# Optimization experiments

Measured on AMD Instinct MI355X. Metric: run time of the kernel, lower is better.

## Reference

```python
import jax, jax.numpy as jnp
import numpy as np

# camera / raster constants
N = 10000            # gaussians
W = 256
H = 256
FX = 200.0
FY = 200.0
TILE = 16
NTX = W // TILE
NTY = H // TILE
NT = NTX * NTY       # 256 tiles
P = TILE * TILE      # 256 pixels per tile
K = 256              # max gaussians kept per tile
NEAR = 0.3
MAGIC = 1.2          # frustum expansion factor from project_culling
LP = 0.3 / (FX * FX) # low-pass filter added to 2D covariance diagonal


def quat_to_rot(q):
    w, x, y, z = q[:, 0], q[:, 1], q[:, 2], q[:, 3]
    r0 = jnp.stack([1 - 2 * (y * y + z * z), 2 * (x * y - w * z), 2 * (x * z + w * y)], -1)
    r1 = jnp.stack([2 * (x * y + w * z), 1 - 2 * (x * x + z * z), 2 * (y * z - w * x)], -1)
    r2 = jnp.stack([2 * (x * z - w * y), 2 * (y * z + w * x), 1 - 2 * (x * x + y * y)], -1)
    return jnp.stack([r0, r1, r2], axis=1)  # [N,3,3]


def splat_forward(pos, rgb, opacity, quaternion, scale, w2c_r, w2c_t):
    # ---- project + frustum cull (global_culling) ----
    q = quaternion / jnp.linalg.norm(quaternion, axis=-1, keepdims=True)
    R = quat_to_rot(q)
    sigma = jnp.exp(scale)                               # normalize_scale
    cov3d = jnp.einsum('nij,nj,nkj->nik', R, sigma * sigma, R)
    p_cam = pos @ w2c_r.T + w2c_t                        # [N,3]
    x, y, z = p_cam[:, 0], p_cam[:, 1], p_cam[:, 2]
    zc = jnp.maximum(z, 1e-6)
    half_w = W * MAGIC / 2 / FX
    half_h = H * MAGIC / 2 / FY
    mean2d = jnp.stack([x / zc, y / zc], -1)             # camera-plane coords
    in_frustum = (z > NEAR) & (jnp.abs(mean2d[:, 0]) < half_w) & (jnp.abs(mean2d[:, 1]) < half_h)
    iz = 1.0 / zc
    zero = jnp.zeros_like(iz)
    J = jnp.stack([jnp.stack([iz, zero, -x * iz * iz], -1),
                   jnp.stack([zero, iz, -y * iz * iz], -1)], axis=1)  # [N,2,3]
    cov_cam = jnp.einsum('ij,njk,lk->nil', w2c_r, cov3d, w2c_r)
    cov2d = jnp.einsum('nij,njk,nlk->nil', J, cov_cam, J)            # [N,2,2]
    a = cov2d[:, 0, 0] + LP
    c = cov2d[:, 1, 1] + LP
    b = cov2d[:, 0, 1]

    # ---- per-tile culling + fixed-K binning (calc_tile_list / gather_gaussians) ----
    cx = (jnp.arange(NTX) * TILE + TILE / 2 - W / 2) / FX
    cy = (jnp.arange(NTY) * TILE + TILE / 2 - H / 2) / FY
    centers = jnp.stack(jnp.meshgrid(cx, cy, indexing='xy'), -1).reshape(NT, 2)  # [NT,2] (ty-major)
    tile_half_diag = 0.5 * jnp.sqrt((TILE / FX) ** 2 + (TILE / FY) ** 2)
    mid = 0.5 * (a + c)
    sigma_max = jnp.sqrt(jnp.maximum(mid + jnp.sqrt(jnp.maximum((0.5 * (a - c)) ** 2 + b * b, 0.0)), 1e-12))
    dist = jnp.linalg.norm(centers[:, None, :] - mean2d[None, :, :], axis=-1)   # [NT,N]
    valid = in_frustum[None, :] & (dist <= (3.0 * sigma_max + tile_half_diag)[None, :])
    score = jnp.where(valid, -dist, -1e10)
    vals, idx = jax.lax.top_k(score, K)                                          # [NT,K]
    valid_k = vals > -1e9

    mean_g = mean2d[idx]                     # [NT,K,2]
    z_g = z[idx]
    a_g, b_g, c_g = a[idx], b[idx], c[idx]
    opa_g = jax.nn.sigmoid(opacity)[idx]
    rgb_g = jax.nn.sigmoid(rgb)[idx]         # [NT,K,3]

    # ---- depth sort within each tile ----
    order = jnp.argsort(jnp.where(valid_k, z_g, jnp.inf), axis=-1)
    def srt(arr):
        o = order.reshape(order.shape + (1,) * (arr.ndim - 2))
        return jnp.take_along_axis(arr, o, axis=1)
    mean_s, a_s, b_s, c_s = srt(mean_g), srt(a_g), srt(b_g), srt(c_g)
    opa_s, rgb_s = srt(opa_g), srt(rgb_g)
    valid_s = srt(valid_k).astype(pos.dtype)

    # ---- per-pixel front-to-back alpha compositing (draw) ----
    px = ((jnp.arange(W) + 0.5 - W / 2) / FX).reshape(NTX, TILE)
    py = ((jnp.arange(H) + 0.5 - H / 2) / FY).reshape(NTY, TILE)
    U = jnp.broadcast_to(px[None, :, None, :], (NTY, NTX, TILE, TILE)).reshape(NT, P)
    V = jnp.broadcast_to(py[:, None, :, None], (NTY, NTX, TILE, TILE)).reshape(NT, P)
    dx = U[:, :, None] - mean_s[:, None, :, 0]          # [NT,P,K]
    dy = V[:, :, None] - mean_s[:, None, :, 1]
    det = jnp.maximum(a_s * c_s - b_s * b_s, 1e-12)[:, None, :]
    maha = (c_s[:, None, :] * dx * dx - 2.0 * b_s[:, None, :] * dx * dy + a_s[:, None, :] * dy * dy) / det
    alpha = jnp.clip(opa_s[:, None, :] * jnp.exp(-0.5 * maha), 0.0, 0.99) * valid_s[:, None, :]
    trans = jnp.cumprod(1.0 - alpha, axis=-1)
    texc = jnp.concatenate([jnp.ones_like(trans[..., :1]), trans[..., :-1]], axis=-1)
    color = jnp.einsum('tpk,tkc->tpc', alpha * texc, rgb_s)  # [NT,P,3]
    img = color.reshape(NTY, NTX, TILE, TILE, 3).transpose(0, 2, 1, 3, 4).reshape(H, W, 3)
    return jnp.clip(img, 0.0, 1.0)


def setup_inputs() -> dict:
    key = jax.random.key(0)
    ks = jax.random.split(key, 6)
    zpos = jax.random.uniform(ks[0], (N,), minval=2.0, maxval=6.0)
    uv = jax.random.uniform(ks[1], (N, 2), minval=-0.6, maxval=0.6)
    pos = jnp.concatenate([uv * zpos[:, None], zpos[:, None]], axis=-1)
    rgb = jax.random.normal(ks[2], (N, 3))              # pre-sigmoid logits
    opacity = jax.random.normal(ks[3], (N,)) + 1.5      # sigmoid -> ~0.8 like init_opacity
    quaternion = jax.random.normal(ks[4], (N, 4))
    scale = 0.2 * jax.random.normal(ks[5], (N, 3)) - 4.5  # exp -> ~0.01 world sigma
    w2c_r = jnp.eye(3, dtype=jnp.float32)
    w2c_t = jnp.zeros((3,), dtype=jnp.float32)
    return {"pos": pos, "rgb": rgb, "opacity": opacity, "quaternion": quaternion,
            "scale": scale, "w2c_r": w2c_r, "w2c_t": w2c_t}


def reference(pos, rgb, opacity, quaternion, scale, w2c_r, w2c_t):
    return splat_forward(pos, rgb, opacity, quaternion, scale, w2c_r, w2c_t)
```

## Files before the change

### kernel.cpp

```cpp
#include <hip/hip_runtime.h>
#include <math.h>

namespace {
constexpr int W = 256, H = 256, TILE = 16, NTX = 16, NT = 256, K = 256;
constexpr float FX = 200.0f, FY = 200.0f, NEARP = 0.3f, MAGIC = 1.2f;
constexpr float LP = 0.3f / (FX * FX);
constexpr float HALF_W = W * MAGIC / 2.0f / FX;
constexpr float HALF_H = H * MAGIC / 2.0f / FY;
constexpr float THDIAG = 0.05656854249492381f;
constexpr int CAP = 2048;
constexpr int N_PAD = 10240;
constexpr int BT = 1024;
constexpr int NB_MAX = 64;
constexpr int SEG = 256;
constexpr size_t A_OFF  = 0;
constexpr size_t B_OFF  = A_OFF + (size_t)N_PAD * 16;
constexpr size_t C_OFF  = B_OFF + (size_t)N_PAD * 16;
constexpr size_t SL_OFF = C_OFF + (size_t)N_PAD * 16;
constexpr size_t LD_OFF = SL_OFF + (size_t)NT * NB_MAX * 4;
constexpr size_t LZ_OFF = LD_OFF + (size_t)NT * NB_MAX * SEG * 8;
constexpr size_t WS_FULL = LZ_OFF + (size_t)NT * NB_MAX * SEG * 8;
}

struct Pre { float mx, my, z, a, b, c, radius; };

__device__ inline Pre preprocess(int g, const float* __restrict__ pos,
                                 const float* __restrict__ quat,
                                 const float* __restrict__ scl,
                                 const float* __restrict__ w2cr,
                                 const float* __restrict__ w2ct) {
  float p0 = pos[3*g+0], p1 = pos[3*g+1], p2 = pos[3*g+2];
  float qw = quat[4*g+0], qx = quat[4*g+1], qy = quat[4*g+2], qz = quat[4*g+3];
  float inv = 1.0f / sqrtf(qw*qw + qx*qx + qy*qy + qz*qz);
  qw *= inv; qx *= inv; qy *= inv; qz *= inv;
  float r00 = 1.f-2.f*(qy*qy+qz*qz), r01 = 2.f*(qx*qy-qw*qz), r02 = 2.f*(qx*qz+qw*qy);
  float r10 = 2.f*(qx*qy+qw*qz), r11 = 1.f-2.f*(qx*qx+qz*qz), r12 = 2.f*(qy*qz-qw*qx);
  float r20 = 2.f*(qx*qz-qw*qy), r21 = 2.f*(qy*qz+qw*qx), r22 = 1.f-2.f*(qx*qx+qy*qy);
  float e0 = expf(scl[3*g+0]); float s0 = e0*e0;
  float e1 = expf(scl[3*g+1]); float s1 = e1*e1;
  float e2 = expf(scl[3*g+2]); float s2 = e2*e2;
  float C00 = r00*r00*s0 + r01*r01*s1 + r02*r02*s2;
  float C01 = r00*r10*s0 + r01*r11*s1 + r02*r12*s2;
  float C02 = r00*r20*s0 + r01*r21*s1 + r02*r22*s2;
  float C11 = r10*r10*s0 + r11*r11*s1 + r12*r12*s2;
  float C12 = r10*r20*s0 + r11*r21*s1 + r12*r22*s2;
  float C22 = r20*r20*s0 + r21*r21*s1 + r22*r22*s2;
  float w00=w2cr[0],w01=w2cr[1],w02=w2cr[2];
  float w10=w2cr[3],w11=w2cr[4],w12=w2cr[5];
  float w20=w2cr[6],w21=w2cr[7],w22=w2cr[8];
  float x = w00*p0 + w01*p1 + w02*p2 + w2ct[0];
  float y = w10*p0 + w11*p1 + w12*p2 + w2ct[1];
  float z = w20*p0 + w21*p1 + w22*p2 + w2ct[2];
  float m00 = w00*C00 + w01*C01 + w02*C02;
  float m01 = w00*C01 + w01*C11 + w02*C12;
  float m02 = w00*C02 + w01*C12 + w02*C22;
  float m10 = w10*C00 + w11*C01 + w12*C02;
  float m11 = w10*C01 + w11*C11 + w12*C12;
  float m12 = w10*C02 + w11*C12 + w12*C22;
  float m20 = w20*C00 + w21*C01 + w22*C02;
  float m21 = w20*C01 + w21*C11 + w22*C12;
  float m22 = w20*C02 + w21*C12 + w22*C22;
  float v00 = m00*w00 + m01*w01 + m02*w02;
  float v01 = m00*w10 + m01*w11 + m02*w12;
  float v02 = m00*w20 + m01*w21 + m02*w22;
  float v10 = m10*w00 + m11*w01 + m12*w02;
  float v11 = m10*w10 + m11*w11 + m12*w12;
  float v12 = m10*w20 + m11*w21 + m12*w22;
  float v20 = m20*w00 + m21*w01 + m22*w02;
  float v21 = m20*w10 + m21*w11 + m22*w12;
  float v22 = m20*w20 + m21*w21 + m22*w22;
  float zc = fmaxf(z, 1e-6f);
  float iz = 1.0f / zc;
  float mx = x * iz, my = y * iz;
  float iz2 = iz * iz;
  float jx = -x * iz2, jy = -y * iz2;
  float a00 = iz*v00 + jx*v20, a01 = iz*v01 + jx*v21, a02 = iz*v02 + jx*v22;
  float a10 = iz*v10 + jy*v20, a11 = iz*v11 + jy*v21, a12 = iz*v12 + jy*v22;
  float A  = a00*iz + a02*jx + LP;
  float Bv = a01*iz + a02*jy;
  float Cv = a11*iz + a12*jy + LP;
  float mid = 0.5f*(A + Cv);
  float hh  = 0.5f*(A - Cv);
  float disc = fmaxf(hh*hh + Bv*Bv, 0.0f);
  float smax = sqrtf(fmaxf(mid + sqrtf(disc), 1e-12f));
  bool infr = (z > NEARP) && (fabsf(mx) < HALF_W) && (fabsf(my) < HALF_H);
  Pre r;
  r.mx = mx; r.my = my; r.z = z; r.a = A; r.b = Bv; r.c = Cv;
  r.radius = infr ? (3.0f * smax + THDIAG) : -1.0f;
  return r;
}


template <bool BIN>
__global__ __launch_bounds__(256)
void pre_bin(const float* __restrict__ pos, const float* __restrict__ rgb,
             const float* __restrict__ opac, const float* __restrict__ quat,
             const float* __restrict__ scl, const float* __restrict__ w2cr,
             const float* __restrict__ w2ct,
             float4* __restrict__ pa, float4* __restrict__ pb,
             float4* __restrict__ pc, int* __restrict__ seglen,
             unsigned long long* __restrict__ listd,
             unsigned long long* __restrict__ listz, int n) {
  __shared__ int s_tc[NT];
  const int tid = (int)threadIdx.x;
  const int blk = (int)blockIdx.x;
  if (BIN) {
    if (tid < NT) s_tc[tid] = 0;
    __syncthreads();
  }
  const int g = blk * 256 + tid;
  if (g < n) {
    Pre p = preprocess(g, pos, quat, scl, w2cr, w2ct);
    float det = fmaxf(p.a * p.c - p.b * p.b, 1e-12f);
    pa[g] = make_float4(p.mx, p.my, p.radius, p.z);
    pb[g] = make_float4(p.a, p.b, p.c, 1.0f / det);
    pc[g] = make_float4(1.0f / (1.0f + __expf(-opac[g])),
                        1.0f / (1.0f + __expf(-rgb[3*g+0])),
                        1.0f / (1.0f + __expf(-rgb[3*g+1])),
                        1.0f / (1.0f + __expf(-rgb[3*g+2])));
    if (BIN && p.radius >= 0.0f) {
      float r = p.radius;
      int txlo = max(0,     (int)floorf(((p.mx - r) * FX + 120.0f) * 0.0625f));
      int txhi = min(NTX-1, (int)ceilf (((p.mx + r) * FX + 120.0f) * 0.0625f));
      int tylo = max(0,     (int)floorf(((p.my - r) * FY + 120.0f) * 0.0625f));
      int tyhi = min(NTX-1, (int)ceilf (((p.my + r) * FY + 120.0f) * 0.0625f));
      unsigned long long gbits = (unsigned int)g;
      for (int ty = tylo; ty <= tyhi; ++ty) {
        float cy = (ty * TILE + TILE * 0.5f - H * 0.5f) / FY;
        float ddy = cy - p.my;
        for (int tx = txlo; tx <= txhi; ++tx) {
          float cx = (tx * TILE + TILE * 0.5f - W * 0.5f) / FX;
          float ddx = cx - p.mx;
          float dist = sqrtf(ddx * ddx + ddy * ddy);
          if (dist <= r) {
            int t = ty * NTX + tx;
            int slot = atomicAdd(&s_tc[t], 1);
            size_t idx = ((size_t)t * NB_MAX + blk) * SEG + slot;
            listd[idx] = ((unsigned long long)__float_as_uint(dist) << 32) | gbits;
            listz[idx] = ((unsigned long long)__float_as_uint(p.z)  << 32) | gbits;
          }
        }
      }
    }
  }
  if (BIN) {
    __syncthreads();
    if (tid < NT) seglen[(size_t)tid * NB_MAX + blk] = s_tc[tid];
  }
}


template <int S>
__device__ inline void hsortN(unsigned long long* key, int M) {
  const int tid = (int)threadIdx.x;
  __syncthreads();
  unsigned long long e[S];
  #pragma unroll
  for (int s = 0; s < S; ++s) {
    int i = tid + (s << 10);
    e[s] = (i < M) ? key[i] : ~0ull;
  }
  for (int k = 2; k <= M; k <<= 1) {
    for (int j = k >> 1; j >= 64; j >>= 1) {
      __syncthreads();
      #pragma unroll
      for (int s = 0; s < S; ++s) {
        int i = tid + (s << 10);
        if (i < M) key[i] = e[s];
      }
      __syncthreads();
      #pragma unroll
      for (int s = 0; s < S; ++s) {
        int i = tid + (s << 10);
        if (i < M) {
          unsigned long long p = key[i ^ j];
          bool takeMin = (((i & j) == 0) == ((i & k) == 0));
          e[s] = ((p < e[s]) == takeMin) ? p : e[s];
        }
      }
    }
    int j0 = ((k >> 1) < 32) ? (k >> 1) : 32;
    for (int j = j0; j >= 1; j >>= 1) {
      #pragma unroll
      for (int s = 0; s < S; ++s) {
        int i = tid + (s << 10);
        unsigned long long p = __shfl_xor(e[s], j, 64);
        bool takeMin = (((i & j) == 0) == ((i & k) == 0));
        e[s] = ((p < e[s]) == takeMin) ? p : e[s];
      }
    }
  }
  __syncthreads();
  #pragma unroll
  for (int s = 0; s < S; ++s) {
    int i = tid + (s << 10);
    if (i < M) key[i] = e[s];
  }
  __syncthreads();
}


__device__ inline void sort_blend_store(
    const float4* __restrict__ pa, const float4* __restrict__ pb,
    const float4* __restrict__ pc, float* __restrict__ out,
    unsigned long long* s_zkey, int* s_rank,
    float4* s_p0, float4* s_p1, float2* s_p2, float4* s_part,
    int cnt2, int tx, int ty) {
  const int tid = (int)threadIdx.x;
  {
    const int e = tid & 255;
    const int q = tid >> 8;
    if (e < cnt2) {
      unsigned long long mykey = s_zkey[e];
      int jlo = q * 64;
      int jhi = min(cnt2, jlo + 64);
      int partial = 0;
      for (int j = jlo; j < jhi; ++j)
        partial += (s_zkey[j] < mykey) ? 1 : 0;
      if (partial) atomicAdd(&s_rank[e], partial);
    }
  }
  __syncthreads();
  if (tid < cnt2) {
    int g = (int)(s_zkey[tid] & 0xffffffffu);
    int r = s_rank[tid];
    float4 A = pa[g], B = pb[g], C = pc[g];
    s_p0[r] = make_float4(A.x, A.y, B.x, B.y);
    s_p1[r] = make_float4(B.z, B.w, C.x, C.y);
    s_p2[r] = make_float2(C.z, C.w);
  }
  __syncthreads();
  const int p    = tid & 255;
  const int q    = tid >> 8;
  const int prow = p / TILE, pcol = p % TILE;
  const float u = ((float)(tx * TILE + pcol) + 0.5f - W * 0.5f) / FX;
  const float v = ((float)(ty * TILE + prow) + 0.5f - H * 0.5f) / FY;
  const int chunk = (cnt2 + 3) >> 2;
  const int k0 = q * chunk;
  const int k1 = min(cnt2, k0 + chunk);
  float T = 1.0f, accr = 0.0f, accg = 0.0f, accb = 0.0f;
  for (int k2 = k0; k2 < k1; ++k2) {
    float4 p0 = s_p0[k2];
    float4 p1 = s_p1[k2];
    float2 p2 = s_p2[k2];
    float dx = u - p0.x;
    float dy = v - p0.y;
    float maha = (p1.x*dx*dx - 2.0f*p0.w*dx*dy + p0.z*dy*dy) * p1.y;
    float alpha = fminf(p1.z * __expf(-0.5f * maha), 0.99f);
    float w = alpha * T;
    accr += w * p1.w;
    accg += w * p2.x;
    accb += w * p2.y;
    T *= (1.0f - alpha);
  }
  s_part[tid] = make_float4(accr, accg, accb, T);
  __syncthreads();
  if (q == 0) {
    float4 P0 = s_part[p];
    float4 P1 = s_part[p + 256];
    float4 P2 = s_part[p + 512];
    float4 P3 = s_part[p + 768];
    float r = P0.x + P0.w * (P1.x + P1.w * (P2.x + P2.w * P3.x));
    float g = P0.y + P0.w * (P1.y + P1.w * (P2.y + P2.w * P3.y));
    float b = P0.z + P0.w * (P1.z + P1.w * (P2.z + P2.w * P3.z));
    const int row = ty * TILE + prow;
    const int col = tx * TILE + pcol;
    const int o = (row * W + col) * 3;
    out[o+0] = fminf(fmaxf(r, 0.0f), 1.0f);
    out[o+1] = fminf(fmaxf(g, 0.0f), 1.0f);
    out[o+2] = fminf(fmaxf(b, 0.0f), 1.0f);
  }
}


__global__ __launch_bounds__(BT)
void render_list(const float4* __restrict__ pa, const float4* __restrict__ pb,
                 const float4* __restrict__ pc, const int* __restrict__ seglen,
                 const unsigned long long* __restrict__ listd,
                 const unsigned long long* __restrict__ listz,
                 float* __restrict__ out, int nb) {
  __shared__ unsigned long long s_dkey[CAP];
  __shared__ unsigned long long s_zkey[CAP];
  __shared__ int s_off[NB_MAX + 1];
  __shared__ int s_rank[K];
  __shared__ float4 s_p0[K];
  __shared__ float4 s_p1[K];
  __shared__ float2 s_p2[K];
  __shared__ float4 s_part[BT];

  const int t  = (int)blockIdx.x;
  const int tx = t % NTX;
  const int ty = t / NTX;
  const int tid = (int)threadIdx.x;

  if (tid < K) s_rank[tid] = 0;
  if (tid < 64) {
    int v = (tid < nb) ? seglen[(size_t)t * NB_MAX + tid] : 0;
    #pragma unroll
    for (int d = 1; d < 64; d <<= 1) {
      int u2 = __shfl_up(v, d, 64);
      if (tid >= d) v += u2;
    }
    if (tid == 0) s_off[0] = 0;
    if (tid < nb) s_off[tid + 1] = v;
  }
  __syncthreads();
  int cnt = min(s_off[nb], CAP);

  for (int i = tid; i < cnt; i += BT) {
    int lo = 0, hi = nb;
    while (hi - lo > 1) {
      int mid = (lo + hi) >> 1;
      if (s_off[mid] <= i) lo = mid; else hi = mid;
    }
    size_t src = ((size_t)t * NB_MAX + lo) * SEG + (size_t)(i - s_off[lo]);
    s_dkey[i] = listd[src];
    s_zkey[i] = listz[src];
  }
  __syncthreads();
  int cnt2 = cnt;

  if (cnt > K) {
    int M = 512; while (M < cnt) M <<= 1;
    for (int i = cnt + tid; i < M; i += BT) s_dkey[i] = ~0ull;
    if (M <= 1024) hsortN<1>(s_dkey, M);
    else           hsortN<2>(s_dkey, 2048);
    if (tid < K) {
      int g = (int)(s_dkey[tid] & 0xffffffffu);
      s_zkey[tid] = ((unsigned long long)__float_as_uint(pa[g].w) << 32) |
                    (unsigned int)g;
    }
    __syncthreads();
    cnt2 = K;
  }

  sort_blend_store(pa, pb, pc, out, s_zkey, s_rank, s_p0, s_p1, s_p2, s_part,
                   cnt2, tx, ty);
}


__global__ __launch_bounds__(BT)
void render_scan(const float4* __restrict__ pa, const float4* __restrict__ pb,
                 const float4* __restrict__ pc, float* __restrict__ out, int n) {
  __shared__ unsigned long long s_dkey[CAP];
  __shared__ unsigned long long s_zkey[CAP];
  __shared__ int s_rank[K];
  __shared__ float4 s_p0[K];
  __shared__ float4 s_p1[K];
  __shared__ float2 s_p2[K];
  __shared__ float4 s_part[BT];
  __shared__ int s_cnt;

  const int t  = (int)blockIdx.x;
  const int tx = t % NTX;
  const int ty = t / NTX;
  const int tid = (int)threadIdx.x;
  const int lane = tid & 63;
  const float cxc = (tx * TILE + TILE * 0.5f - W * 0.5f) / FX;
  const float cyc = (ty * TILE + TILE * 0.5f - H * 0.5f) / FY;

  if (tid == 0) s_cnt = 0;
  if (tid < K) s_rank[tid] = 0;
  __syncthreads();

  for (int g = tid; g < n; g += BT) {
    float4 v = pa[g];
    float ddx = cxc - v.x, ddy = cyc - v.y;
    float dist = sqrtf(ddx * ddx + ddy * ddy);
    bool hit = (v.z >= 0.0f) && (dist <= v.z);
    unsigned long long m = __ballot(hit);
    if (m) {
      int leader = __ffsll((long long)m) - 1;
      int base = 0;
      if (lane == leader) base = atomicAdd(&s_cnt, __popcll(m));
      base = __shfl(base, leader, 64);
      if (hit) {
        int slot = base + __popcll(m & ((1ull << lane) - 1ull));
        if (slot < CAP) {
          s_dkey[slot] = ((unsigned long long)__float_as_uint(dist) << 32) |
                         (unsigned int)g;
          s_zkey[slot] = ((unsigned long long)__float_as_uint(v.w) << 32) |
                         (unsigned int)g;
        }
      }
    }
  }
  __syncthreads();
  int cnt = min(s_cnt, CAP);
  int cnt2 = cnt;

  if (cnt > K) {
    int M = 512; while (M < cnt) M <<= 1;
    for (int i = cnt + tid; i < M; i += BT) s_dkey[i] = ~0ull;
    if (M <= 1024) hsortN<1>(s_dkey, M);
    else           hsortN<2>(s_dkey, 2048);
    if (tid < K) {
      int g = (int)(s_dkey[tid] & 0xffffffffu);
      s_zkey[tid] = ((unsigned long long)__float_as_uint(pa[g].w) << 32) |
                    (unsigned int)g;
    }
    __syncthreads();
    cnt2 = K;
  }

  sort_blend_store(pa, pb, pc, out, s_zkey, s_rank, s_p0, s_p1, s_p2, s_part,
                   cnt2, tx, ty);
}

extern "C" void kernel_launch(void* const* d_in, const int* in_sizes, int n_in,
                              void* d_out, int out_size, void* d_ws, size_t ws_size,
                              hipStream_t stream) {
  const float* pos  = (const float*)d_in[0];
  const float* rgb  = (const float*)d_in[1];
  const float* opac = (const float*)d_in[2];
  const float* quat = (const float*)d_in[3];
  const float* scl  = (const float*)d_in[4];
  const float* w2cr = (const float*)d_in[5];
  const float* w2ct = (const float*)d_in[6];
  float* out = (float*)d_out;
  const int n = in_sizes[0] / 3;
  const int nb = (n + 255) / 256;

  char* ws = (char*)d_ws;
  float4* pa = (float4*)(ws + A_OFF);
  float4* pb = (float4*)(ws + B_OFF);
  float4* pc = (float4*)(ws + C_OFF);
  int* seglen = (int*)(ws + SL_OFF);
  unsigned long long* listd = (unsigned long long*)(ws + LD_OFF);
  unsigned long long* listz = (unsigned long long*)(ws + LZ_OFF);

  if (ws_size >= WS_FULL && nb <= NB_MAX) {
    pre_bin<true><<<nb, 256, 0, stream>>>(
        pos, rgb, opac, quat, scl, w2cr, w2ct, pa, pb, pc, seglen, listd, listz, n);
    render_list<<<NT, BT, 0, stream>>>(pa, pb, pc, seglen, listd, listz, out, nb);
  } else {
    pre_bin<false><<<nb, 256, 0, stream>>>(
        pos, rgb, opac, quat, scl, w2cr, w2ct, pa, pb, pc, seglen, listd, listz, n);
    render_scan<<<NT, BT, 0, stream>>>(pa, pb, pc, out, n);
  }
}
```

Measured before the change: 24.99 us.

## Fuse preprocess/binning and tile render into one cooperative kernel with grid sync

```diff
diff --git a/kernel.cpp b/kernel.cpp
--- a/kernel.cpp
+++ b/kernel.cpp
@@ -1,5 +1,8 @@
 #include <hip/hip_runtime.h>
+#include <hip/hip_cooperative_groups.h>
 #include <math.h>
+
+namespace cg = cooperative_groups;
 
 namespace {
 constexpr int W = 256, H = 256, TILE = 16, NTX = 16, NT = 256, K = 256;
@@ -8,7 +11,7 @@
 constexpr float HALF_W = W * MAGIC / 2.0f / FX;
 constexpr float HALF_H = H * MAGIC / 2.0f / FY;
 constexpr float THDIAG = 0.05656854249492381f;
-constexpr int CAP = 2048;
+constexpr int CAP = 1024;
 constexpr int N_PAD = 10240;
 constexpr int BT = 1024;
 constexpr int NB_MAX = 64;
@@ -90,117 +93,83 @@
   return r;
 }
 
-
 template <bool BIN>
-__global__ __launch_bounds__(256)
-void pre_bin(const float* __restrict__ pos, const float* __restrict__ rgb,
-             const float* __restrict__ opac, const float* __restrict__ quat,
-             const float* __restrict__ scl, const float* __restrict__ w2cr,
-             const float* __restrict__ w2ct,
-             float4* __restrict__ pa, float4* __restrict__ pb,
-             float4* __restrict__ pc, int* __restrict__ seglen,
-             unsigned long long* __restrict__ listd,
-             unsigned long long* __restrict__ listz, int n) {
-  __shared__ int s_tc[NT];
-  const int tid = (int)threadIdx.x;
-  const int blk = (int)blockIdx.x;
-  if (BIN) {
-    if (tid < NT) s_tc[tid] = 0;
-    __syncthreads();
-  }
-  const int g = blk * 256 + tid;
-  if (g < n) {
-    Pre p = preprocess(g, pos, quat, scl, w2cr, w2ct);
-    float det = fmaxf(p.a * p.c - p.b * p.b, 1e-12f);
-    pa[g] = make_float4(p.mx, p.my, p.radius, p.z);
-    pb[g] = make_float4(p.a, p.b, p.c, 1.0f / det);
-    pc[g] = make_float4(1.0f / (1.0f + __expf(-opac[g])),
-                        1.0f / (1.0f + __expf(-rgb[3*g+0])),
-                        1.0f / (1.0f + __expf(-rgb[3*g+1])),
-                        1.0f / (1.0f + __expf(-rgb[3*g+2])));
-    if (BIN && p.radius >= 0.0f) {
-      float r = p.radius;
-      int txlo = max(0,     (int)floorf(((p.mx - r) * FX + 120.0f) * 0.0625f));
-      int txhi = min(NTX-1, (int)ceilf (((p.mx + r) * FX + 120.0f) * 0.0625f));
-      int tylo = max(0,     (int)floorf(((p.my - r) * FY + 120.0f) * 0.0625f));
-      int tyhi = min(NTX-1, (int)ceilf (((p.my + r) * FY + 120.0f) * 0.0625f));
-      unsigned long long gbits = (unsigned int)g;
-      for (int ty = tylo; ty <= tyhi; ++ty) {
-        float cy = (ty * TILE + TILE * 0.5f - H * 0.5f) / FY;
-        float ddy = cy - p.my;
-        for (int tx = txlo; tx <= txhi; ++tx) {
-          float cx = (tx * TILE + TILE * 0.5f - W * 0.5f) / FX;
-          float ddx = cx - p.mx;
-          float dist = sqrtf(ddx * ddx + ddy * ddy);
-          if (dist <= r) {
-            int t = ty * NTX + tx;
-            int slot = atomicAdd(&s_tc[t], 1);
-            size_t idx = ((size_t)t * NB_MAX + blk) * SEG + slot;
-            listd[idx] = ((unsigned long long)__float_as_uint(dist) << 32) | gbits;
-            listz[idx] = ((unsigned long long)__float_as_uint(p.z)  << 32) | gbits;
-          }
+__device__ inline void pre_one(int g, int blk, const float* __restrict__ pos,
+                               const float* __restrict__ rgb,
+                               const float* __restrict__ opac,
+                               const float* __restrict__ quat,
+                               const float* __restrict__ scl,
+                               const float* __restrict__ w2cr,
+                               const float* __restrict__ w2ct,
+                               float4* __restrict__ pa, float4* __restrict__ pb,
+                               float4* __restrict__ pc,
+                               unsigned long long* __restrict__ listd,
+                               unsigned long long* __restrict__ listz,
+                               int* s_tc) {
+  Pre p = preprocess(g, pos, quat, scl, w2cr, w2ct);
+  float det = fmaxf(p.a * p.c - p.b * p.b, 1e-12f);
+  pa[g] = make_float4(p.mx, p.my, p.radius, p.z);
+  pb[g] = make_float4(p.a, p.b, p.c, 1.0f / det);
+  pc[g] = make_float4(1.0f / (1.0f + __expf(-opac[g])),
+                      1.0f / (1.0f + __expf(-rgb[3*g+0])),
+                      1.0f / (1.0f + __expf(-rgb[3*g+1])),
+                      1.0f / (1.0f + __expf(-rgb[3*g+2])));
+  if (BIN && p.radius >= 0.0f) {
+    float r = p.radius;
+    int txlo = max(0,     (int)floorf(((p.mx - r) * FX + 120.0f) * 0.0625f));
+    int txhi = min(NTX-1, (int)ceilf (((p.mx + r) * FX + 120.0f) * 0.0625f));
+    int tylo = max(0,     (int)floorf(((p.my - r) * FY + 120.0f) * 0.0625f));
+    int tyhi = min(NTX-1, (int)ceilf (((p.my + r) * FY + 120.0f) * 0.0625f));
+    unsigned long long gbits = (unsigned int)g;
+    for (int ty = tylo; ty <= tyhi; ++ty) {
+      float cy = (ty * TILE + TILE * 0.5f - H * 0.5f) / FY;
+      float ddy = cy - p.my;
+      for (int tx = txlo; tx <= txhi; ++tx) {
+        float cx = (tx * TILE + TILE * 0.5f - W * 0.5f) / FX;
+        float ddx = cx - p.mx;
+        float dist = sqrtf(ddx * ddx + ddy * ddy);
+        if (dist <= r) {
+          int t = ty * NTX + tx;
+          int slot = atomicAdd(&s_tc[t], 1);
+          size_t idx = ((size_t)t * NB_MAX + blk) * SEG + slot;
+          listd[idx] = ((unsigned long long)__float_as_uint(dist) << 32) | gbits;
+          listz[idx] = ((unsigned long long)__float_as_uint(p.z)  << 32) | gbits;
         }
       }
     }
   }
-  if (BIN) {
-    __syncthreads();
-    if (tid < NT) seglen[(size_t)tid * NB_MAX + blk] = s_tc[tid];
-  }
-}
-
-
-template <int S>
-__device__ inline void hsortN(unsigned long long* key, int M) {
+}
+
+
+__device__ inline void hsort1(unsigned long long* key, int M) {
   const int tid = (int)threadIdx.x;
   __syncthreads();
-  unsigned long long e[S];
-  #pragma unroll
-  for (int s = 0; s < S; ++s) {
-    int i = tid + (s << 10);
-    e[s] = (i < M) ? key[i] : ~0ull;
-  }
+  unsigned long long e = (tid < M) ? key[tid] : ~0ull;
   for (int k = 2; k <= M; k <<= 1) {
     for (int j = k >> 1; j >= 64; j >>= 1) {
       __syncthreads();
-      #pragma unroll
-      for (int s = 0; s < S; ++s) {
-        int i = tid + (s << 10);
-        if (i < M) key[i] = e[s];
-      }
+      if (tid < M) key[tid] = e;
       __syncthreads();
-      #pragma unroll
-      for (int s = 0; s < S; ++s) {
-        int i = tid + (s << 10);
-        if (i < M) {
-          unsigned long long p = key[i ^ j];
-          bool takeMin = (((i & j) == 0) == ((i & k) == 0));
-          e[s] = ((p < e[s]) == takeMin) ? p : e[s];
-        }
+      if (tid < M) {
+        unsigned long long p = key[tid ^ j];
+        bool takeMin = (((tid & j) == 0) == ((tid & k) == 0));
+        e = ((p < e) == takeMin) ? p : e;
       }
     }
     int j0 = ((k >> 1) < 32) ? (k >> 1) : 32;
     for (int j = j0; j >= 1; j >>= 1) {
-      #pragma unroll
-      for (int s = 0; s < S; ++s) {
-        int i = tid + (s << 10);
-        unsigned long long p = __shfl_xor(e[s], j, 64);
-        bool takeMin = (((i & j) == 0) == ((i & k) == 0));
-        e[s] = ((p < e[s]) == takeMin) ? p : e[s];
-      }
-    }
-  }
-  __syncthreads();
-  #pragma unroll
-  for (int s = 0; s < S; ++s) {
-    int i = tid + (s << 10);
-    if (i < M) key[i] = e[s];
-  }
-  __syncthreads();
-}
-
-
-__device__ inline void sort_blend_store(
+      unsigned long long p = __shfl_xor(e, j, 64);
+      bool takeMin = (((tid & j) == 0) == ((tid & k) == 0));
+      e = ((p < e) == takeMin) ? p : e;
+    }
+  }
+  __syncthreads();
+  if (tid < M) key[tid] = e;
+  __syncthreads();
+}
+
+
+__device__ inline void tail_blend(
     const float4* __restrict__ pa, const float4* __restrict__ pb,
     const float4* __restrict__ pc, float* __restrict__ out,
     unsigned long long* s_zkey, int* s_rank,
@@ -274,13 +243,18 @@
 
 
 __global__ __launch_bounds__(BT)
-void render_list(const float4* __restrict__ pa, const float4* __restrict__ pb,
-                 const float4* __restrict__ pc, const int* __restrict__ seglen,
-                 const unsigned long long* __restrict__ listd,
-                 const unsigned long long* __restrict__ listz,
-                 float* __restrict__ out, int nb) {
+void splat_fused(const float* __restrict__ pos, const float* __restrict__ rgb,
+                 const float* __restrict__ opac, const float* __restrict__ quat,
+                 const float* __restrict__ scl, const float* __restrict__ w2cr,
+                 const float* __restrict__ w2ct,
+                 float4* __restrict__ pa, float4* __restrict__ pb,
+                 float4* __restrict__ pc, int* __restrict__ seglen,
+                 unsigned long long* __restrict__ listd,
+                 unsigned long long* __restrict__ listz,
+                 float* __restrict__ out, int n, int nb) {
+  __shared__ int s_tc[NT];
+  __shared__ unsigned long long s_zkey[CAP];
   __shared__ unsigned long long s_dkey[CAP];
-  __shared__ unsigned long long s_zkey[CAP];
   __shared__ int s_off[NB_MAX + 1];
   __shared__ int s_rank[K];
   __shared__ float4 s_p0[K];
@@ -288,10 +262,25 @@
   __shared__ float2 s_p2[K];
   __shared__ float4 s_part[BT];
 
-  const int t  = (int)blockIdx.x;
+  const int blk = (int)blockIdx.x;
+  const int tid = (int)threadIdx.x;
+
+  if (blk < nb && tid < NT) s_tc[tid] = 0;
+  __syncthreads();
+  if (blk < nb && tid < 256) {
+    int g = blk * 256 + tid;
+    if (g < n)
+      pre_one<true>(g, blk, pos, rgb, opac, quat, scl, w2cr, w2ct,
+                    pa, pb, pc, listd, listz, s_tc);
+  }
+  __syncthreads();
+  if (blk < nb && tid < NT) seglen[(size_t)tid * NB_MAX + blk] = s_tc[tid];
+
+  cg::this_grid().sync();
+
+  const int t  = blk;
   const int tx = t % NTX;
   const int ty = t / NTX;
-  const int tid = (int)threadIdx.x;
 
   if (tid < K) s_rank[tid] = 0;
   if (tid < 64) {
@@ -314,17 +303,24 @@
       if (s_off[mid] <= i) lo = mid; else hi = mid;
     }
     size_t src = ((size_t)t * NB_MAX + lo) * SEG + (size_t)(i - s_off[lo]);
-    s_dkey[i] = listd[src];
     s_zkey[i] = listz[src];
   }
   __syncthreads();
   int cnt2 = cnt;
 
   if (cnt > K) {
+    for (int i = tid; i < cnt; i += BT) {
+      int lo = 0, hi = nb;
+      while (hi - lo > 1) {
+        int mid = (lo + hi) >> 1;
+        if (s_off[mid] <= i) lo = mid; else hi = mid;
+      }
+      size_t src = ((size_t)t * NB_MAX + lo) * SEG + (size_t)(i - s_off[lo]);
+      s_dkey[i] = listd[src];
+    }
     int M = 512; while (M < cnt) M <<= 1;
     for (int i = cnt + tid; i < M; i += BT) s_dkey[i] = ~0ull;
-    if (M <= 1024) hsortN<1>(s_dkey, M);
-    else           hsortN<2>(s_dkey, 2048);
+    hsort1(s_dkey, M);
     if (tid < K) {
       int g = (int)(s_dkey[tid] & 0xffffffffu);
       s_zkey[tid] = ((unsigned long long)__float_as_uint(pa[g].w) << 32) |
@@ -334,16 +330,29 @@
     cnt2 = K;
   }
 
-  sort_blend_store(pa, pb, pc, out, s_zkey, s_rank, s_p0, s_p1, s_p2, s_part,
-                   cnt2, tx, ty);
-}
-
+  tail_blend(pa, pb, pc, out, s_zkey, s_rank, s_p0, s_p1, s_p2, s_part,
+             cnt2, tx, ty);
+}
+
+
+__global__ __launch_bounds__(256)
+void pre_only(const float* __restrict__ pos, const float* __restrict__ rgb,
+              const float* __restrict__ opac, const float* __restrict__ quat,
+              const float* __restrict__ scl, const float* __restrict__ w2cr,
+              const float* __restrict__ w2ct,
+              float4* __restrict__ pa, float4* __restrict__ pb,
+              float4* __restrict__ pc, int n) {
+  int g = blockIdx.x * 256 + (int)threadIdx.x;
+  if (g >= n) return;
+  pre_one<false>(g, 0, pos, rgb, opac, quat, scl, w2cr, w2ct,
+                 pa, pb, pc, nullptr, nullptr, nullptr);
+}
 
 __global__ __launch_bounds__(BT)
 void render_scan(const float4* __restrict__ pa, const float4* __restrict__ pb,
                  const float4* __restrict__ pc, float* __restrict__ out, int n) {
+  __shared__ unsigned long long s_zkey[CAP];
   __shared__ unsigned long long s_dkey[CAP];
-  __shared__ unsigned long long s_zkey[CAP];
   __shared__ int s_rank[K];
   __shared__ float4 s_p0[K];
   __shared__ float4 s_p1[K];
@@ -392,8 +401,7 @@
   if (cnt > K) {
     int M = 512; while (M < cnt) M <<= 1;
     for (int i = cnt + tid; i < M; i += BT) s_dkey[i] = ~0ull;
-    if (M <= 1024) hsortN<1>(s_dkey, M);
-    else           hsortN<2>(s_dkey, 2048);
+    hsort1(s_dkey, M);
     if (tid < K) {
       int g = (int)(s_dkey[tid] & 0xffffffffu);
       s_zkey[tid] = ((unsigned long long)__float_as_uint(pa[g].w) << 32) |
@@ -403,8 +411,8 @@
     cnt2 = K;
   }
 
-  sort_blend_store(pa, pb, pc, out, s_zkey, s_rank, s_p0, s_p1, s_p2, s_part,
-                   cnt2, tx, ty);
+  tail_blend(pa, pb, pc, out, s_zkey, s_rank, s_p0, s_p1, s_p2, s_part,
+             cnt2, tx, ty);
 }
 
 extern "C" void kernel_launch(void* const* d_in, const int* in_sizes, int n_in,
@@ -418,8 +426,8 @@
   const float* w2cr = (const float*)d_in[5];
   const float* w2ct = (const float*)d_in[6];
   float* out = (float*)d_out;
-  const int n = in_sizes[0] / 3;
-  const int nb = (n + 255) / 256;
+  int n = in_sizes[0] / 3;
+  int nb = (n + 255) / 256;
 
   char* ws = (char*)d_ws;
   float4* pa = (float4*)(ws + A_OFF);
@@ -430,12 +438,16 @@
   unsigned long long* listz = (unsigned long long*)(ws + LZ_OFF);
 
   if (ws_size >= WS_FULL && nb <= NB_MAX) {
-    pre_bin<true><<<nb, 256, 0, stream>>>(
-        pos, rgb, opac, quat, scl, w2cr, w2ct, pa, pb, pc, seglen, listd, listz, n);
-    render_list<<<NT, BT, 0, stream>>>(pa, pb, pc, seglen, listd, listz, out, nb);
+    void* args[] = {(void*)&pos, (void*)&rgb, (void*)&opac, (void*)&quat,
+                    (void*)&scl, (void*)&w2cr, (void*)&w2ct,
+                    (void*)&pa, (void*)&pb, (void*)&pc, (void*)&seglen,
+                    (void*)&listd, (void*)&listz, (void*)&out,
+                    (void*)&n, (void*)&nb};
+    hipLaunchCooperativeKernel(reinterpret_cast<void*>(splat_fused),
+                               dim3(NT), dim3(BT), args, 0, stream);
   } else {
-    pre_bin<false><<<nb, 256, 0, stream>>>(
-        pos, rgb, opac, quat, scl, w2cr, w2ct, pa, pb, pc, seglen, listd, listz, n);
+    pre_only<<<nb, 256, 0, stream>>>(pos, rgb, opac, quat, scl, w2cr, w2ct,
+                                     pa, pb, pc, n);
     render_scan<<<NT, BT, 0, stream>>>(pa, pb, pc, out, n);
   }
 }
```

Result: slower. 51.93 us (+107.8%).
